# Kernel tuning notes

Measured on AMD Instinct MI355X. Metric: run time of the kernel, lower is better.

Reference implementation:

```python
import jax, jax.numpy as jnp
import numpy as np

TEMP = 1.0  # softmax temperature from init_kwargs
NEG_BIG = -1e8


def setup_inputs() -> dict:
    key = jax.random.key(0)
    ks = jax.random.split(key, 7)
    T, S, B, H, C, M = 128, 128, 32, 512, 512, 256
    return {
        "hid": jax.random.normal(ks[0], (T, B, H), dtype=jnp.float32),
        "ctx": jax.random.normal(ks[1], (S, B, C), dtype=jnp.float32),
        "ctx_mask": jnp.ones((S, B), dtype=jnp.float32),
        "W_hid2mid": jax.random.normal(ks[2], (M, H), dtype=jnp.float32) * 0.05,
        "W_ctx2mid": jax.random.normal(ks[3], (M, C), dtype=jnp.float32) * 0.05,
        "w_ff": jax.random.normal(ks[4], (M,), dtype=jnp.float32) * 0.05,
        "W_att2hid": jax.random.normal(ks[5], (H, C), dtype=jnp.float32) * 0.05,
    }


def reference(hid, ctx, ctx_mask, W_hid2mid, W_ctx2mid, w_ff, W_att2hid):
    # hid: (T,B,H)  ctx: (S,B,C)  ctx_mask: (S,B)
    hid_m = jnp.einsum('tbh,mh->tbm', hid, W_hid2mid)   # (T,B,M)
    ctx_m = jnp.einsum('sbc,mc->sbm', ctx, W_ctx2mid)   # (S,B,M)
    # broadcast-add -> (S,T,B,M), tanh, project with ff (mid->1), -> scores (S,B,T)
    summed = jnp.tanh(hid_m[None, :, :, :] + ctx_m[:, None, :, :])
    scores = jnp.einsum('stbm,m->sbt', summed, w_ff) / TEMP
    # masked_fill where ctx_mask == 0
    scores = jnp.where(ctx_mask[:, :, None] > 0, scores, NEG_BIG)
    alpha = jax.nn.softmax(scores, axis=0)              # (S,B,T), softmax over S
    attended = jnp.einsum('sbt,sbc->tbc', alpha, ctx)   # (T,B,C)
    z_t = jnp.einsum('tbc,hc->tbh', attended, W_att2hid)  # (T,B,H)
    # torch returns alpha.permute(1,2,0) of (B,T,S) => (T,S,B)
    return (jnp.transpose(alpha, (2, 0, 1)), z_t)
```

## Files before the change

kernel.cpp:

```cpp
#include <hip/hip_runtime.h>
#include <hip/hip_bf16.h>

#define T_DIM 128
#define S_DIM 128
#define B_DIM 32
#define H_DIM 512
#define C_DIM 512
#define M_DIM 256
#define NEG_BIG -1e8f
#define K2LOG2E 2.8853900817779268f

typedef __attribute__((ext_vector_type(8))) short shortx8;
typedef __attribute__((ext_vector_type(4))) float floatx4;

__device__ __forceinline__ unsigned bfpair(float a, float b) {
  unsigned ua = __builtin_bit_cast(unsigned, a); ua += 0x7fffu + ((ua >> 16) & 1u);
  unsigned ub = __builtin_bit_cast(unsigned, b); ub += 0x7fffu + ((ub >> 16) & 1u);
  return (ua >> 16) | (ub & 0xffff0000u);
}
__device__ __forceinline__ uint4 pack2(const float4& a, const float4& b) {
  uint4 o;
  o.x = bfpair(a.x, a.y); o.y = bfpair(a.z, a.w);
  o.z = bfpair(b.x, b.y); o.w = bfpair(b.z, b.w);
  return o;
}
__device__ __forceinline__ ushort bf1(float a) {
  unsigned ua = __builtin_bit_cast(unsigned, a); ua += 0x7fffu + ((ua >> 16) & 1u);
  return (ushort)(ua >> 16);
}

__device__ __forceinline__ void cvt8(const float* __restrict__ s,
                                     ushort* __restrict__ d, int g) {
  const float4 x = *(const float4*)(s + (size_t)g * 8);
  const float4 y = *(const float4*)(s + (size_t)g * 8 + 4);
  uint4 o;
  o.x = bfpair(x.x, x.y); o.y = bfpair(x.z, x.w);
  o.z = bfpair(y.x, y.y); o.w = bfpair(y.z, y.w);
  *(uint4*)(d + (size_t)g * 8) = o;
}

__global__ __launch_bounds__(256) void cvt_kernel(
    const float* a0, ushort* b0, int c0, const float* a1, ushort* b1, int c1,
    const float* a2, ushort* b2, int c2, const float* a3, ushort* b3, int c3,
    const float* a4, ushort* b4, int c4) {
  int g = blockIdx.x * 256 + threadIdx.x;
  if (g < c0) { cvt8(a0, b0, g); return; } g -= c0;
  if (g < c1) { cvt8(a1, b1, g); return; } g -= c1;
  if (g < c2) { cvt8(a2, b2, g); return; } g -= c2;
  if (g < c3) { cvt8(a3, b3, g); return; } g -= c3;
  if (g < c4) { cvt8(a4, b4, g); }
}

__device__ __forceinline__ void gemm_core_bf16(
    const ushort* __restrict__ X, const ushort* __restrict__ W,
    int n0, int m0, int K, int nk, ushort* Xs, ushort* Ws, int tid,
    floatx4 acc[2][2]) {
  const int lane = tid & 63;
  const int wave = tid >> 6, wn = wave & 1, wm = wave >> 1;
  const int l15 = lane & 15, lhi = lane >> 4;
  const int r = tid >> 3, c8 = tid & 7;
  const int sw0 = (c8 ^ (r & 7)) << 4;
  char* xr0 = (char*)Xs + r * 128 + sw0;
  char* xr1 = (char*)Xs + (r + 32) * 128 + sw0;
  char* wr0 = (char*)Ws + r * 128 + sw0;
  char* wr1 = (char*)Ws + (r + 32) * 128 + sw0;

  const ushort* xp0 = X + (size_t)(n0 + r) * K + c8 * 8;
  const ushort* xp1 = xp0 + (size_t)32 * K;
  const ushort* wp0 = W + (size_t)(m0 + r) * K + c8 * 8;
  const ushort* wp1 = wp0 + (size_t)32 * K;

  uint4 xu0 = *(const uint4*)xp0, xu1 = *(const uint4*)xp1;
  uint4 wu0 = *(const uint4*)wp0, wu1 = *(const uint4*)wp1;

  for (int it = 0; it < nk; ++it) {
    __syncthreads();
    *(uint4*)xr0 = xu0; *(uint4*)xr1 = xu1;
    *(uint4*)wr0 = wu0; *(uint4*)wr1 = wu1;
    __syncthreads();
    if (it + 1 < nk) {
      xp0 += 64; xp1 += 64; wp0 += 64; wp1 += 64;
      xu0 = *(const uint4*)xp0; xu1 = *(const uint4*)xp1;
      wu0 = *(const uint4*)wp0; wu1 = *(const uint4*)wp1;
    }
#pragma unroll
    for (int ks = 0; ks < 2; ++ks) {
      const int slot = lhi + (ks << 2);
      shortx8 af[2], bfr[2];
#pragma unroll
      for (int fi = 0; fi < 2; ++fi) {
        const int row = wn * 32 + fi * 16 + l15;
        af[fi] = *(const shortx8*)((const char*)Xs + row * 128 + ((slot ^ (row & 7)) << 4));
      }
#pragma unroll
      for (int fj = 0; fj < 2; ++fj) {
        const int col = wm * 32 + fj * 16 + l15;
        bfr[fj] = *(const shortx8*)((const char*)Ws + col * 128 + ((slot ^ (col & 7)) << 4));
      }
#pragma unroll
      for (int fi = 0; fi < 2; ++fi)
#pragma unroll
        for (int fj = 0; fj < 2; ++fj)
          acc[fi][fj] = __builtin_amdgcn_mfma_f32_16x16x32_bf16(af[fi], bfr[fj], acc[fi][fj], 0, 0, 0);
    }
  }
}

__global__ __launch_bounds__(256) void gemm_multi(
    const ushort* __restrict__ HB, const ushort* __restrict__ WhB, float* __restrict__ EH,
    const ushort* __restrict__ CB, const ushort* __restrict__ WcB, float* __restrict__ EC,
    const ushort* __restrict__ WaB, ushort* __restrict__ CWT) {
  __shared__ ushort Xs[4096];
  __shared__ ushort Ws[4096];
  const int tid = threadIdx.x;
  const int bid = blockIdx.x;

  const ushort *X, *W;
  int n0, m0;
  if (bid < 512) {
    const int lb = bid & 255;
    n0 = (lb >> 2) << 6; m0 = (lb & 3) << 6;
    X = (bid < 256) ? HB : CB;
    W = (bid < 256) ? WhB : WcB;
  } else {
    const int lb = bid - 512;
    n0 = (lb >> 3) << 6;
    m0 = (lb & 7) << 6;
    X = CB;
    W = WaB;
  }

  floatx4 acc[2][2];
#pragma unroll
  for (int i = 0; i < 2; ++i)
#pragma unroll
    for (int j = 0; j < 2; ++j) acc[i][j] = (floatx4){0.f, 0.f, 0.f, 0.f};

  gemm_core_bf16(X, W, n0, m0, 512, 8, Xs, Ws, tid, acc);

  const int lane = tid & 63, wave = tid >> 6;
  const int wn = wave & 1, wm = wave >> 1;
  const int l15 = lane & 15, lhi = lane >> 4;
  if (bid < 512) {
    float* Y = (bid < 256) ? EH : EC;
#pragma unroll
    for (int fi = 0; fi < 2; ++fi)
#pragma unroll
      for (int fj = 0; fj < 2; ++fj)
#pragma unroll
        for (int r = 0; r < 4; ++r) {
          const int row = n0 + wn * 32 + fi * 16 + lhi * 4 + r;
          const int col = m0 + wm * 32 + fj * 16 + l15;
          Y[(size_t)row * M_DIM + col] = __builtin_amdgcn_exp2f(K2LOG2E * acc[fi][fj][r]);
        }
  } else {
#pragma unroll
    for (int fi = 0; fi < 2; ++fi)
#pragma unroll
      for (int fj = 0; fj < 2; ++fj)
#pragma unroll
        for (int r = 0; r < 4; ++r) {
          const int row = n0 + wn * 32 + fi * 16 + lhi * 4 + r;
          const int col = m0 + wm * 32 + fj * 16 + l15;
          CWT[(size_t)row * H_DIM + col] = bf1(acc[fi][fj][r]);
        }
  }
}

__global__ __launch_bounds__(256) void zgemm_kernel(
    const float* __restrict__ AWS, const ushort* __restrict__ CWT,
    float* __restrict__ z) {
  __shared__ ushort Xs[4096];
  __shared__ ushort WsT[64 * 72];
  const int tid = threadIdx.x;
  const int m0 = blockIdx.x << 6;
  const int n0 = blockIdx.y << 6;
  const int b = blockIdx.z;
  const int lane = tid & 63, wave = tid >> 6;
  const int wn = wave & 1, wm = wave >> 1;
  const int l15 = lane & 15, lhi = lane >> 4;
  const int r = tid >> 3, c8 = tid & 7;
  const int lr = tid & 63, ls = tid >> 6;
  const int sw0 = (c8 ^ (r & 7)) << 4;
  char* xr0 = (char*)Xs + r * 128 + sw0;
  char* xr1 = (char*)Xs + (r + 32) * 128 + sw0;

  float4 xa[2][2], xb[2][2];
  uint4 wv[2][2];
#pragma unroll
  for (int it = 0; it < 2; ++it) {
    const float* p0 = AWS + ((size_t)(n0 + r) * B_DIM + b) * S_DIM + it * 64 + c8 * 8;
    const float* p1 = AWS + ((size_t)(n0 + r + 32) * B_DIM + b) * S_DIM + it * 64 + c8 * 8;
    xa[it][0] = ((const float4*)p0)[0]; xa[it][1] = ((const float4*)p0)[1];
    xb[it][0] = ((const float4*)p1)[0]; xb[it][1] = ((const float4*)p1)[1];
    const ushort* q = CWT + ((size_t)(it * 64 + lr) * B_DIM + b) * H_DIM + m0 + ls * 8;
    wv[it][0] = *(const uint4*)q;
    wv[it][1] = *(const uint4*)(q + 32);
  }

  floatx4 acc[2][2];
#pragma unroll
  for (int i = 0; i < 2; ++i)
#pragma unroll
    for (int j = 0; j < 2; ++j) acc[i][j] = (floatx4){0.f, 0.f, 0.f, 0.f};

#pragma unroll
  for (int it = 0; it < 2; ++it) {
    __syncthreads();
    *(uint4*)xr0 = pack2(xa[it][0], xa[it][1]);
    *(uint4*)xr1 = pack2(xb[it][0], xb[it][1]);
#pragma unroll
    for (int q = 0; q < 2; ++q) {
      const int hb = ls * 8 + q * 32;
      const ushort* vs = (const ushort*)&wv[it][q];
#pragma unroll
      for (int i = 0; i < 8; ++i) WsT[(hb + i) * 72 + lr] = vs[i];
    }
    __syncthreads();
#pragma unroll
    for (int ks = 0; ks < 2; ++ks) {
      const int slot = lhi + (ks << 2);
      shortx8 af[2], bfr[2];
#pragma unroll
      for (int fi = 0; fi < 2; ++fi) {
        const int row = wn * 32 + fi * 16 + l15;
        af[fi] = *(const shortx8*)((const char*)Xs + row * 128 + ((slot ^ (row & 7)) << 4));
      }
#pragma unroll
      for (int fj = 0; fj < 2; ++fj) {
        const int col = wm * 32 + fj * 16 + l15;
        bfr[fj] = *(const shortx8*)((const char*)WsT + col * 144 + (slot << 4));
      }
#pragma unroll
      for (int fi = 0; fi < 2; ++fi)
#pragma unroll
        for (int fj = 0; fj < 2; ++fj)
          acc[fi][fj] = __builtin_amdgcn_mfma_f32_16x16x32_bf16(af[fi], bfr[fj], acc[fi][fj], 0, 0, 0);
    }
  }

#pragma unroll
  for (int fi = 0; fi < 2; ++fi)
#pragma unroll
    for (int fj = 0; fj < 2; ++fj)
#pragma unroll
      for (int r2 = 0; r2 < 4; ++r2) {
        const int t = n0 + wn * 32 + fi * 16 + lhi * 4 + r2;
        const int h = m0 + wm * 32 + fj * 16 + l15;
        z[((size_t)t * B_DIM + b) * H_DIM + h] = acc[fi][fj][r2];
      }
}

__global__ __launch_bounds__(256) void scores_kernel(
    const float* __restrict__ EH, const float* __restrict__ EC,
    const float* __restrict__ w_ff, const float* __restrict__ ctx_mask,
    float* __restrict__ aws) {
  __shared__ float4 ec[2][8][128];
  __shared__ float4 eh[2][8][8];
  __shared__ float4 wf[2][8];
  __shared__ float msk[S_DIM];
  const int tid = threadIdx.x;
  const int b = blockIdx.y;
  const int t0 = blockIdx.x << 3;
  const int tt = tid >> 6;
  const int st = tid & 63;

  if (tid < S_DIM) msk[tid] = ctx_mask[(size_t)tid * B_DIM + b];

  float4 rec[4], reh, rwf;
#define SLOAD(C)                                                                \
  {                                                                             \
    _Pragma("unroll")                                                           \
    for (int i = 0; i < 4; ++i) {                                               \
      const int idx = tid + (i << 8);                                           \
      const int s_ = idx >> 3, q_ = idx & 7;                                    \
      rec[i] = *(const float4*)(EC + ((size_t)s_ * B_DIM + b) * M_DIM + ((C) << 5) + (q_ << 2)); \
    }                                                                           \
    if (tid < 64)                                                               \
      reh = *(const float4*)(EH + ((size_t)(t0 + (tid >> 3)) * B_DIM + b) * M_DIM + ((C) << 5) + ((tid & 7) << 2)); \
    if (tid < 8) rwf = *(const float4*)(w_ff + ((C) << 5) + (tid << 2));        \
  }
#define SSTORE(BUF)                                                             \
  {                                                                             \
    _Pragma("unroll")                                                           \
    for (int i = 0; i < 4; ++i) {                                               \
      const int idx = tid + (i << 8);                                           \
      ec[BUF][idx & 7][idx >> 3] = rec[i];                                      \
    }                                                                           \
    if (tid < 64) eh[BUF][tid & 7][tid >> 3] = reh;                             \
    if (tid < 8) wf[BUF][tid] = rwf;                                            \
  }

  floatx4 acc[2][2];
#pragma unroll
  for (int i = 0; i < 2; ++i)
#pragma unroll
    for (int j = 0; j < 2; ++j) acc[i][j] = (floatx4){0.f, 0.f, 0.f, 0.f};

  SLOAD(0)
  SSTORE(0)
  __syncthreads();

  for (int c = 0; c < 8; ++c) {
    const int cur = c & 1;
    if (c < 7) SLOAD(c + 1)
#pragma unroll
    for (int q = 0; q < 8; ++q) {
      const float4 w4 = wf[cur][q];
      const float4 e0 = eh[cur][q][2 * tt], e1 = eh[cur][q][2 * tt + 1];
      const float4 c0 = ec[cur][q][st],     c1 = ec[cur][q][st + 64];
#define ACC1(A, E, Cc)                                                 \
  A[0] += w4.x * __builtin_amdgcn_rcpf(E.x * Cc.x + 1.f);              \
  A[1] += w4.y * __builtin_amdgcn_rcpf(E.y * Cc.y + 1.f);              \
  A[2] += w4.z * __builtin_amdgcn_rcpf(E.z * Cc.z + 1.f);              \
  A[3] += w4.w * __builtin_amdgcn_rcpf(E.w * Cc.w + 1.f);
      ACC1(acc[0][0], e0, c0) ACC1(acc[0][1], e0, c1)
      ACC1(acc[1][0], e1, c0) ACC1(acc[1][1], e1, c1)
#undef ACC1
    }
    if (c < 7) {
      SSTORE(cur ^ 1)
      __syncthreads();
    }
  }
#undef SLOAD
#undef SSTORE

  const float mk0 = msk[st], mk1 = msk[st + 64];
  float sc[2][2];
#pragma unroll
  for (int ti = 0; ti < 2; ++ti) {
    const floatx4 a0 = acc[ti][0], a1 = acc[ti][1];
    sc[ti][0] = (mk0 > 0.f) ? -2.f * (a0[0] + a0[1] + a0[2] + a0[3]) : NEG_BIG;
    sc[ti][1] = (mk1 > 0.f) ? -2.f * (a1[0] + a1[1] + a1[2] + a1[3]) : NEG_BIG;
  }
#pragma unroll
  for (int ti = 0; ti < 2; ++ti) {
    float mx = fmaxf(sc[ti][0], sc[ti][1]);
#pragma unroll
    for (int off = 32; off > 0; off >>= 1) mx = fmaxf(mx, __shfl_xor(mx, off));
    const float e0 = __expf(sc[ti][0] - mx), e1 = __expf(sc[ti][1] - mx);
    float sum = e0 + e1;
#pragma unroll
    for (int off = 32; off > 0; off >>= 1) sum += __shfl_xor(sum, off);
    const float rinv = 1.f / sum;
    float* w = aws + ((size_t)(t0 + 2 * tt + ti) * B_DIM + b) * S_DIM;
    w[st] = e0 * rinv;
    w[st + 64] = e1 * rinv;
  }
}

__global__ __launch_bounds__(256) void alpha_tr_kernel(
    const float* __restrict__ aws, float* __restrict__ aout) {
  __shared__ float al[32][129];
  const int t = blockIdx.x;
  const int tid = threadIdx.x;
  {
    const int b_ = tid >> 3, q = tid & 7;
    const float* src = aws + ((size_t)t * B_DIM + b_) * S_DIM + q * 16;
#pragma unroll
    for (int i = 0; i < 4; ++i)
      *(float4*)&al[b_][q * 16 + i * 4] = ((const float4*)src)[i];
  }
  __syncthreads();
  {
    const int s = tid >> 1, half = tid & 1;
    float* dst = aout + ((size_t)t * S_DIM + s) * B_DIM + half * 16;
#pragma unroll
    for (int i = 0; i < 4; ++i) {
      float4 o;
      o.x = al[half * 16 + i * 4 + 0][s];
      o.y = al[half * 16 + i * 4 + 1][s];
      o.z = al[half * 16 + i * 4 + 2][s];
      o.w = al[half * 16 + i * 4 + 3][s];
      ((float4*)dst)[i] = o;
    }
  }
}

extern "C" void kernel_launch(void* const* d_in, const int* in_sizes, int n_in,
                              void* d_out, int out_size, void* d_ws, size_t ws_size,
                              hipStream_t stream) {
  const float* hid       = (const float*)d_in[0];
  const float* ctx       = (const float*)d_in[1];
  const float* ctx_mask  = (const float*)d_in[2];
  const float* W_hid2mid = (const float*)d_in[3];
  const float* W_ctx2mid = (const float*)d_in[4];
  const float* w_ff      = (const float*)d_in[5];
  const float* W_att2hid = (const float*)d_in[6];
  float* out = (float*)d_out;
  float* ws  = (float*)d_ws;

  const size_t MEG = 1 << 20;
  float*  EH  = ws;
  float*  EC  = ws + MEG;
  float*  AWS = ws + 2 * MEG;
  ushort* CWT = (ushort*)(ws + 2 * MEG + MEG / 2);
  ushort* HB  = (ushort*)(ws + 4 * MEG);
  ushort* CB  = (ushort*)(ws + 5 * MEG);
  ushort* WhB = (ushort*)(ws + 6 * MEG);
  ushort* WcB = WhB + 131072;
  ushort* WaB = WcB + 131072;
  float* alpha_out = out;
  float* z_out     = out + T_DIM * S_DIM * B_DIM;

  dim3 blk(256);
  cvt_kernel<<<2304, blk, 0, stream>>>(hid, HB, 262144, ctx, CB, 262144,
                                       W_hid2mid, WhB, 16384, W_ctx2mid, WcB, 16384,
                                       W_att2hid, WaB, 32768);
  gemm_multi<<<1024, blk, 0, stream>>>(HB, WhB, EH, CB, WcB, EC, WaB, CWT);
  scores_kernel<<<dim3(T_DIM / 8, B_DIM), blk, 0, stream>>>(EH, EC, w_ff, ctx_mask, AWS);
  alpha_tr_kernel<<<T_DIM, blk, 0, stream>>>(AWS, alpha_out);
  zgemm_kernel<<<dim3(H_DIM / 64, T_DIM / 64, B_DIM), blk, 0, stream>>>(AWS, CWT, z_out);
}
```

Measured before the change: 60.53 us.

## Fuse fp32-to-bf16 activation conversion into GEMM loads and enlarge tiles to 128x128

The separate conversion of hid and ctx to bf16 is dropped. The GEMM now reads the fp32 activations directly and packs them to bf16 while storing to shared memory, which removes one full write and re-read of the activation buffers. The GEMM tile also grows from 64x64 to 128x128 with a 4x4 MFMA fragment grid per wave, so fewer blocks (256 instead of 1024) each do more reuse. The cost is more registers, fewer blocks to fill the CUs, and twice the global bytes per activation load inside the GEMM.

```diff
diff --git a/kernel.cpp b/kernel.cpp
--- a/kernel.cpp
+++ b/kernel.cpp
@@ -41,128 +41,128 @@
 
 __global__ __launch_bounds__(256) void cvt_kernel(
     const float* a0, ushort* b0, int c0, const float* a1, ushort* b1, int c1,
-    const float* a2, ushort* b2, int c2, const float* a3, ushort* b3, int c3,
-    const float* a4, ushort* b4, int c4) {
+    const float* a2, ushort* b2, int c2) {
   int g = blockIdx.x * 256 + threadIdx.x;
   if (g < c0) { cvt8(a0, b0, g); return; } g -= c0;
   if (g < c1) { cvt8(a1, b1, g); return; } g -= c1;
-  if (g < c2) { cvt8(a2, b2, g); return; } g -= c2;
-  if (g < c3) { cvt8(a3, b3, g); return; } g -= c3;
-  if (g < c4) { cvt8(a4, b4, g); }
-}
-
-__device__ __forceinline__ void gemm_core_bf16(
-    const ushort* __restrict__ X, const ushort* __restrict__ W,
-    int n0, int m0, int K, int nk, ushort* Xs, ushort* Ws, int tid,
-    floatx4 acc[2][2]) {
-  const int lane = tid & 63;
-  const int wave = tid >> 6, wn = wave & 1, wm = wave >> 1;
-  const int l15 = lane & 15, lhi = lane >> 4;
-  const int r = tid >> 3, c8 = tid & 7;
-  const int sw0 = (c8 ^ (r & 7)) << 4;
-  char* xr0 = (char*)Xs + r * 128 + sw0;
-  char* xr1 = (char*)Xs + (r + 32) * 128 + sw0;
-  char* wr0 = (char*)Ws + r * 128 + sw0;
-  char* wr1 = (char*)Ws + (r + 32) * 128 + sw0;
-
-  const ushort* xp0 = X + (size_t)(n0 + r) * K + c8 * 8;
-  const ushort* xp1 = xp0 + (size_t)32 * K;
-  const ushort* wp0 = W + (size_t)(m0 + r) * K + c8 * 8;
-  const ushort* wp1 = wp0 + (size_t)32 * K;
-
-  uint4 xu0 = *(const uint4*)xp0, xu1 = *(const uint4*)xp1;
-  uint4 wu0 = *(const uint4*)wp0, wu1 = *(const uint4*)wp1;
-
-  for (int it = 0; it < nk; ++it) {
-    __syncthreads();
-    *(uint4*)xr0 = xu0; *(uint4*)xr1 = xu1;
-    *(uint4*)wr0 = wu0; *(uint4*)wr1 = wu1;
-    __syncthreads();
-    if (it + 1 < nk) {
-      xp0 += 64; xp1 += 64; wp0 += 64; wp1 += 64;
-      xu0 = *(const uint4*)xp0; xu1 = *(const uint4*)xp1;
-      wu0 = *(const uint4*)wp0; wu1 = *(const uint4*)wp1;
-    }
-#pragma unroll
-    for (int ks = 0; ks < 2; ++ks) {
-      const int slot = lhi + (ks << 2);
-      shortx8 af[2], bfr[2];
-#pragma unroll
-      for (int fi = 0; fi < 2; ++fi) {
-        const int row = wn * 32 + fi * 16 + l15;
-        af[fi] = *(const shortx8*)((const char*)Xs + row * 128 + ((slot ^ (row & 7)) << 4));
-      }
-#pragma unroll
-      for (int fj = 0; fj < 2; ++fj) {
-        const int col = wm * 32 + fj * 16 + l15;
-        bfr[fj] = *(const shortx8*)((const char*)Ws + col * 128 + ((slot ^ (col & 7)) << 4));
-      }
-#pragma unroll
-      for (int fi = 0; fi < 2; ++fi)
-#pragma unroll
-        for (int fj = 0; fj < 2; ++fj)
-          acc[fi][fj] = __builtin_amdgcn_mfma_f32_16x16x32_bf16(af[fi], bfr[fj], acc[fi][fj], 0, 0, 0);
-    }
-  }
+  if (g < c2) { cvt8(a2, b2, g); }
 }
 
 __global__ __launch_bounds__(256) void gemm_multi(
-    const ushort* __restrict__ HB, const ushort* __restrict__ WhB, float* __restrict__ EH,
-    const ushort* __restrict__ CB, const ushort* __restrict__ WcB, float* __restrict__ EC,
+    const float* __restrict__ hid, const ushort* __restrict__ WhB, float* __restrict__ EH,
+    const float* __restrict__ ctx, const ushort* __restrict__ WcB, float* __restrict__ EC,
     const ushort* __restrict__ WaB, ushort* __restrict__ CWT) {
-  __shared__ ushort Xs[4096];
-  __shared__ ushort Ws[4096];
+  __shared__ ushort Xs[128 * 64];
+  __shared__ ushort Ws[128 * 64];
   const int tid = threadIdx.x;
   const int bid = blockIdx.x;
 
-  const ushort *X, *W;
+  const float* X;
+  const ushort* W;
   int n0, m0;
-  if (bid < 512) {
-    const int lb = bid & 255;
-    n0 = (lb >> 2) << 6; m0 = (lb & 3) << 6;
-    X = (bid < 256) ? HB : CB;
-    W = (bid < 256) ? WhB : WcB;
+  if (bid < 128) {
+    const int lb = bid & 63;
+    n0 = (lb >> 1) << 7; m0 = (lb & 1) << 7;
+    X = (bid < 64) ? hid : ctx;
+    W = (bid < 64) ? WhB : WcB;
   } else {
-    const int lb = bid - 512;
-    n0 = (lb >> 3) << 6;
-    m0 = (lb & 7) << 6;
-    X = CB;
+    const int lb = bid - 128;
+    n0 = (lb >> 2) << 7;
+    m0 = (lb & 3) << 7;
+    X = ctx;
     W = WaB;
   }
-
-  floatx4 acc[2][2];
-#pragma unroll
-  for (int i = 0; i < 2; ++i)
-#pragma unroll
-    for (int j = 0; j < 2; ++j) acc[i][j] = (floatx4){0.f, 0.f, 0.f, 0.f};
-
-  gemm_core_bf16(X, W, n0, m0, 512, 8, Xs, Ws, tid, acc);
 
   const int lane = tid & 63, wave = tid >> 6;
   const int wn = wave & 1, wm = wave >> 1;
   const int l15 = lane & 15, lhi = lane >> 4;
-  if (bid < 512) {
-    float* Y = (bid < 256) ? EH : EC;
-#pragma unroll
-    for (int fi = 0; fi < 2; ++fi)
-#pragma unroll
-      for (int fj = 0; fj < 2; ++fj)
-#pragma unroll
-        for (int r = 0; r < 4; ++r) {
-          const int row = n0 + wn * 32 + fi * 16 + lhi * 4 + r;
-          const int col = m0 + wm * 32 + fj * 16 + l15;
-          Y[(size_t)row * M_DIM + col] = __builtin_amdgcn_exp2f(K2LOG2E * acc[fi][fj][r]);
+  const int r = tid >> 3, c8 = tid & 7;
+  const int sw = (c8 ^ (r & 7)) << 4;
+
+  const float* xp[4];
+  const ushort* wp[4];
+  char* xdst[4];
+  char* wdst[4];
+#pragma unroll
+  for (int j = 0; j < 4; ++j) {
+    xp[j] = X + (size_t)(n0 + r + 32 * j) * 512 + c8 * 8;
+    wp[j] = W + (size_t)(m0 + r + 32 * j) * 512 + c8 * 8;
+    xdst[j] = (char*)Xs + (r + 32 * j) * 128 + sw;
+    wdst[j] = (char*)Ws + (r + 32 * j) * 128 + sw;
+  }
+
+  float4 xf[4][2];
+  uint4 wu[4];
+#define LOADXW                                         \
+  _Pragma("unroll")                                    \
+  for (int j = 0; j < 4; ++j) {                        \
+    xf[j][0] = ((const float4*)xp[j])[0];              \
+    xf[j][1] = ((const float4*)xp[j])[1];              \
+    wu[j] = *(const uint4*)wp[j];                      \
+  }
+  LOADXW
+
+  floatx4 acc[4][4];
+#pragma unroll
+  for (int i = 0; i < 4; ++i)
+#pragma unroll
+    for (int j = 0; j < 4; ++j) acc[i][j] = (floatx4){0.f, 0.f, 0.f, 0.f};
+
+  for (int it = 0; it < 8; ++it) {
+    __syncthreads();
+#pragma unroll
+    for (int j = 0; j < 4; ++j) {
+      *(uint4*)xdst[j] = pack2(xf[j][0], xf[j][1]);
+      *(uint4*)wdst[j] = wu[j];
+    }
+    __syncthreads();
+    if (it < 7) {
+#pragma unroll
+      for (int j = 0; j < 4; ++j) { xp[j] += 64; wp[j] += 64; }
+      LOADXW
+    }
+#pragma unroll
+    for (int ks = 0; ks < 2; ++ks) {
+      const int slot = lhi + (ks << 2);
+      const int sws = (slot ^ (l15 & 7)) << 4;
+      shortx8 af[4], bfr[4];
+#pragma unroll
+      for (int fi = 0; fi < 4; ++fi)
+        af[fi] = *(const shortx8*)((const char*)Xs + (wn * 64 + fi * 16 + l15) * 128 + sws);
+#pragma unroll
+      for (int fj = 0; fj < 4; ++fj)
+        bfr[fj] = *(const shortx8*)((const char*)Ws + (wm * 64 + fj * 16 + l15) * 128 + sws);
+#pragma unroll
+      for (int fi = 0; fi < 4; ++fi)
+#pragma unroll
+        for (int fj = 0; fj < 4; ++fj)
+          acc[fi][fj] = __builtin_amdgcn_mfma_f32_16x16x32_bf16(af[fi], bfr[fj], acc[fi][fj], 0, 0, 0);
+    }
+  }
+#undef LOADXW
+
+  if (bid < 128) {
+    float* Y = (bid < 64) ? EH : EC;
+#pragma unroll
+    for (int fi = 0; fi < 4; ++fi)
+#pragma unroll
+      for (int fj = 0; fj < 4; ++fj)
+#pragma unroll
+        for (int rr = 0; rr < 4; ++rr) {
+          const int row = n0 + wn * 64 + fi * 16 + lhi * 4 + rr;
+          const int col = m0 + wm * 64 + fj * 16 + l15;
+          Y[(size_t)row * M_DIM + col] = __builtin_amdgcn_exp2f(K2LOG2E * acc[fi][fj][rr]);
         }
   } else {
 #pragma unroll
-    for (int fi = 0; fi < 2; ++fi)
-#pragma unroll
-      for (int fj = 0; fj < 2; ++fj)
-#pragma unroll
-        for (int r = 0; r < 4; ++r) {
-          const int row = n0 + wn * 32 + fi * 16 + lhi * 4 + r;
-          const int col = m0 + wm * 32 + fj * 16 + l15;
-          CWT[(size_t)row * H_DIM + col] = bf1(acc[fi][fj][r]);
+    for (int fi = 0; fi < 4; ++fi)
+#pragma unroll
+      for (int fj = 0; fj < 4; ++fj)
+#pragma unroll
+        for (int rr = 0; rr < 4; ++rr) {
+          const int row = n0 + wn * 64 + fi * 16 + lhi * 4 + rr;
+          const int col = m0 + wm * 64 + fj * 16 + l15;
+          CWT[(size_t)row * H_DIM + col] = bf1(acc[fi][fj][rr]);
         }
   }
 }
@@ -396,19 +396,17 @@
   float*  EC  = ws + MEG;
   float*  AWS = ws + 2 * MEG;
   ushort* CWT = (ushort*)(ws + 2 * MEG + MEG / 2);
-  ushort* HB  = (ushort*)(ws + 4 * MEG);
-  ushort* CB  = (ushort*)(ws + 5 * MEG);
-  ushort* WhB = (ushort*)(ws + 6 * MEG);
+  ushort* WhB = (ushort*)(ws + 4 * MEG);
   ushort* WcB = WhB + 131072;
   ushort* WaB = WcB + 131072;
   float* alpha_out = out;
   float* z_out     = out + T_DIM * S_DIM * B_DIM;
 
   dim3 blk(256);
-  cvt_kernel<<<2304, blk, 0, stream>>>(hid, HB, 262144, ctx, CB, 262144,
-                                       W_hid2mid, WhB, 16384, W_ctx2mid, WcB, 16384,
-                                       W_att2hid, WaB, 32768);
-  gemm_multi<<<1024, blk, 0, stream>>>(HB, WhB, EH, CB, WcB, EC, WaB, CWT);
+  cvt_kernel<<<256, blk, 0, stream>>>(W_hid2mid, WhB, 16384,
+                                      W_ctx2mid, WcB, 16384,
+                                      W_att2hid, WaB, 32768);
+  gemm_multi<<<256, blk, 0, stream>>>(hid, WhB, EH, ctx, WcB, EC, WaB, CWT);
   scores_kernel<<<dim3(T_DIM / 8, B_DIM), blk, 0, stream>>>(EH, EC, w_ff, ctx_mask, AWS);
   alpha_tr_kernel<<<T_DIM, blk, 0, stream>>>(AWS, alpha_out);
   zgemm_kernel<<<dim3(H_DIM / 64, T_DIM / 64, B_DIM), blk, 0, stream>>>(AWS, CWT, z_out);
```

After: 70.51 us. 16.5% more time.

## Double-buffer GEMM tiles in LDS using direct global-to-LDS loads

Applied to the files above, without the earlier changes.

Replaces the register-staged GEMM main loop with global_load_lds transfers that write bf16 tiles straight into LDS. Two LDS buffers let the next K-slice load while MFMA works on the current one, and the loop needs one barrier per iteration instead of two. This saves VGPRs and barrier stalls, at the cost of doubling LDS use per block. Correctness depends on the per-lane swizzle matching the LDS layout and on the async loads having completed by the time the barrier is reached.

```diff
diff --git a/kernel.cpp b/kernel.cpp
--- a/kernel.cpp
+++ b/kernel.cpp
@@ -28,6 +28,11 @@
   unsigned ua = __builtin_bit_cast(unsigned, a); ua += 0x7fffu + ((ua >> 16) & 1u);
   return (ushort)(ua >> 16);
 }
+
+#define GLDS(G, L)                                                        \
+  __builtin_amdgcn_global_load_lds(                                       \
+      (const __attribute__((address_space(1))) unsigned int*)(G),         \
+      (__attribute__((address_space(3))) unsigned int*)(L), 16, 0, 0)
 
 __device__ __forceinline__ void cvt8(const float* __restrict__ s,
                                      ushort* __restrict__ d, int g) {
@@ -51,67 +56,12 @@
   if (g < c4) { cvt8(a4, b4, g); }
 }
 
-__device__ __forceinline__ void gemm_core_bf16(
-    const ushort* __restrict__ X, const ushort* __restrict__ W,
-    int n0, int m0, int K, int nk, ushort* Xs, ushort* Ws, int tid,
-    floatx4 acc[2][2]) {
-  const int lane = tid & 63;
-  const int wave = tid >> 6, wn = wave & 1, wm = wave >> 1;
-  const int l15 = lane & 15, lhi = lane >> 4;
-  const int r = tid >> 3, c8 = tid & 7;
-  const int sw0 = (c8 ^ (r & 7)) << 4;
-  char* xr0 = (char*)Xs + r * 128 + sw0;
-  char* xr1 = (char*)Xs + (r + 32) * 128 + sw0;
-  char* wr0 = (char*)Ws + r * 128 + sw0;
-  char* wr1 = (char*)Ws + (r + 32) * 128 + sw0;
-
-  const ushort* xp0 = X + (size_t)(n0 + r) * K + c8 * 8;
-  const ushort* xp1 = xp0 + (size_t)32 * K;
-  const ushort* wp0 = W + (size_t)(m0 + r) * K + c8 * 8;
-  const ushort* wp1 = wp0 + (size_t)32 * K;
-
-  uint4 xu0 = *(const uint4*)xp0, xu1 = *(const uint4*)xp1;
-  uint4 wu0 = *(const uint4*)wp0, wu1 = *(const uint4*)wp1;
-
-  for (int it = 0; it < nk; ++it) {
-    __syncthreads();
-    *(uint4*)xr0 = xu0; *(uint4*)xr1 = xu1;
-    *(uint4*)wr0 = wu0; *(uint4*)wr1 = wu1;
-    __syncthreads();
-    if (it + 1 < nk) {
-      xp0 += 64; xp1 += 64; wp0 += 64; wp1 += 64;
-      xu0 = *(const uint4*)xp0; xu1 = *(const uint4*)xp1;
-      wu0 = *(const uint4*)wp0; wu1 = *(const uint4*)wp1;
-    }
-#pragma unroll
-    for (int ks = 0; ks < 2; ++ks) {
-      const int slot = lhi + (ks << 2);
-      shortx8 af[2], bfr[2];
-#pragma unroll
-      for (int fi = 0; fi < 2; ++fi) {
-        const int row = wn * 32 + fi * 16 + l15;
-        af[fi] = *(const shortx8*)((const char*)Xs + row * 128 + ((slot ^ (row & 7)) << 4));
-      }
-#pragma unroll
-      for (int fj = 0; fj < 2; ++fj) {
-        const int col = wm * 32 + fj * 16 + l15;
-        bfr[fj] = *(const shortx8*)((const char*)Ws + col * 128 + ((slot ^ (col & 7)) << 4));
-      }
-#pragma unroll
-      for (int fi = 0; fi < 2; ++fi)
-#pragma unroll
-        for (int fj = 0; fj < 2; ++fj)
-          acc[fi][fj] = __builtin_amdgcn_mfma_f32_16x16x32_bf16(af[fi], bfr[fj], acc[fi][fj], 0, 0, 0);
-    }
-  }
-}
-
 __global__ __launch_bounds__(256) void gemm_multi(
     const ushort* __restrict__ HB, const ushort* __restrict__ WhB, float* __restrict__ EH,
     const ushort* __restrict__ CB, const ushort* __restrict__ WcB, float* __restrict__ EC,
     const ushort* __restrict__ WaB, ushort* __restrict__ CWT) {
-  __shared__ ushort Xs[4096];
-  __shared__ ushort Ws[4096];
+  __shared__ ushort Xs[2][4096];
+  __shared__ ushort Ws[2][4096];
   const int tid = threadIdx.x;
   const int bid = blockIdx.x;
 
@@ -130,17 +80,64 @@
     W = WaB;
   }
 
-  floatx4 acc[2][2];
-#pragma unroll
-  for (int i = 0; i < 2; ++i)
-#pragma unroll
-    for (int j = 0; j < 2; ++j) acc[i][j] = (floatx4){0.f, 0.f, 0.f, 0.f};
-
-  gemm_core_bf16(X, W, n0, m0, 512, 8, Xs, Ws, tid, acc);
-
   const int lane = tid & 63, wave = tid >> 6;
   const int wn = wave & 1, wm = wave >> 1;
   const int l15 = lane & 15, lhi = lane >> 4;
+
+  const int row0 = wave * 16 + (lane >> 3);
+  const int row1 = row0 + 8;
+  const int slot = (lane & 7) ^ (lane >> 3);
+  const ushort* xg0 = X + (size_t)(n0 + row0) * 512 + slot * 8;
+  const ushort* xg1 = X + (size_t)(n0 + row1) * 512 + slot * 8;
+  const ushort* wg0 = W + (size_t)(m0 + row0) * 512 + slot * 8;
+  const ushort* wg1 = W + (size_t)(m0 + row1) * 512 + slot * 8;
+  const int lb0 = wave * 1024;
+  const int lb1 = wave * 1024 + 512;
+
+#define STAGE(NB)                       \
+  {                                     \
+    GLDS(xg0, &Xs[NB][lb0]);            \
+    GLDS(xg1, &Xs[NB][lb1]);            \
+    GLDS(wg0, &Ws[NB][lb0]);            \
+    GLDS(wg1, &Ws[NB][lb1]);            \
+    xg0 += 64; xg1 += 64;               \
+    wg0 += 64; wg1 += 64;               \
+  }
+
+  floatx4 acc[2][2];
+#pragma unroll
+  for (int i = 0; i < 2; ++i)
+#pragma unroll
+    for (int j = 0; j < 2; ++j) acc[i][j] = (floatx4){0.f, 0.f, 0.f, 0.f};
+
+  STAGE(0)
+  __syncthreads();
+  int cur = 0;
+
+  for (int it = 0; it < 8; ++it) {
+    if (it < 7) STAGE(cur ^ 1)
+#pragma unroll
+    for (int ks = 0; ks < 2; ++ks) {
+      const int slotr = lhi + (ks << 2);
+      const int sws = ((slotr ^ (l15 & 7)) << 4);
+      shortx8 af[2], bfr[2];
+#pragma unroll
+      for (int fi = 0; fi < 2; ++fi)
+        af[fi] = *(const shortx8*)((const char*)&Xs[cur][0] + (wn * 32 + fi * 16 + l15) * 128 + sws);
+#pragma unroll
+      for (int fj = 0; fj < 2; ++fj)
+        bfr[fj] = *(const shortx8*)((const char*)&Ws[cur][0] + (wm * 32 + fj * 16 + l15) * 128 + sws);
+#pragma unroll
+      for (int fi = 0; fi < 2; ++fi)
+#pragma unroll
+        for (int fj = 0; fj < 2; ++fj)
+          acc[fi][fj] = __builtin_amdgcn_mfma_f32_16x16x32_bf16(af[fi], bfr[fj], acc[fi][fj], 0, 0, 0);
+    }
+    __syncthreads();
+    cur ^= 1;
+  }
+#undef STAGE
+
   if (bid < 512) {
     float* Y = (bid < 256) ? EH : EC;
 #pragma unroll
```

New measurement: 61.15 us. About the same (+1.0%).
